# Optimization experiments

Hardware: AMD Instinct MI355X
Metric: run time of the kernel (lower is better)

## Reference

```python
import jax, jax.numpy as jnp
import numpy as np

_EPS = 1e-5
_I48 = float(1.0 / np.sqrt(48.0))
_I16 = float(1.0 / np.sqrt(16.0))
# fully-connected TP paths (mul_in, mul_out) for hidden(48x0e+48x1o+16x1e) x sh(0e+1e+2e) -> hidden
_PATHS = [(48, 48), (48, 16), (48, 48), (48, 48), (48, 48), (16, 16), (16, 48), (16, 16), (16, 16)]
_NW = sum(i * o for i, o in _PATHS)  # 11520


def _ln(x, g, b):
    mu = x.mean(-1, keepdims=True)
    var = ((x - mu) ** 2).mean(-1, keepdims=True)
    return g * (x - mu) * jax.lax.rsqrt(var + _EPS) + b


def _split(W):
    out, off = [], 0
    for i, o in _PATHS:
        out.append(W[:, off:off + i * o].reshape(-1, i, o))
        off += i * o
    return out


def _forward(protein_coords, protein_features, ligand_coords, ligand_features, t,
             te_w1, te_b1, te_w2, te_b2, te_ln_g, te_ln_b,
             pe_w1, pe_b1, pe_ln_g, pe_ln_b, pe_w2, pe_b2,
             le_w1, le_b1, le_ln_g, le_ln_b, le_w2, le_b2,
             sp_w, sp_b, emb_w, ee_w1, ee_b1, ee_w2, ee_b2,
             conv_w1, conv_b1, conv_w2, conv_b2, conv_w3, conv_b3,
             bn_gs, bn_bs, bn_gv, bn_gw, si_ws, si_wv, si_ww,
             out_ws, out_wv, edge_src, edge_dst):
    Nl = ligand_coords.shape[0]
    Np = protein_coords.shape[0]
    N = Nl + Np
    E = edge_src.shape[0]
    silu = jax.nn.silu

    # sinusoidal time embedding -> Linear/SiLU/Linear/LayerNorm
    half = 32
    freq = jnp.exp(jnp.arange(half, dtype=jnp.float32) * (-np.log(10000.0) / (half - 1)))
    emb = t[:, None] * freq[None, :]
    emb = jnp.concatenate([jnp.sin(emb), jnp.cos(emb)], -1)  # (1, 64)
    temb = _ln(silu(emb @ te_w1 + te_b1) @ te_w2 + te_b2, te_ln_g, te_ln_b)

    # scalar node encoders (dropout = eval identity)
    protein_ca = protein_coords[:, 0, :]
    ph = silu(_ln(protein_features @ pe_w1 + pe_b1, pe_ln_g, pe_ln_b)) @ pe_w2 + pe_b2
    lh = silu(_ln(ligand_features @ le_w1 + le_b1, le_ln_g, le_ln_b)) @ le_w2 + le_b2

    # edge geometry (ligand -> protein) + spherical harmonics in Cartesian form
    vec = ligand_coords[edge_src] - protein_ca[edge_dst]  # (E, 3)
    dist = jnp.sqrt((vec ** 2).sum(-1) + 1e-12)
    n = vec / dist[:, None]  # unit vector = l=1 SH
    Q = n[:, :, None] * n[:, None, :] - jnp.eye(3, dtype=n.dtype) / 3.0  # l=2 SH (traceless sym)
    te_exp = jnp.broadcast_to(temb[0], (E, temb.shape[-1]))
    ef = silu(jnp.concatenate([dist[:, None], te_exp], -1) @ ee_w1 + ee_b1) @ ee_w2 + ee_b2  # (E, 32)

    # input embedding: scalars only feed 0e; 1o/1e channels start at zero
    comb = jnp.concatenate([lh, ph], 0) @ sp_w + sp_b  # (N, 48)
    s = (comb @ emb_w) * _I48
    v = jnp.zeros((N, 48, 3), s.dtype)
    w = jnp.zeros((N, 16, 3), s.dtype)

    dst_n = edge_dst + Nl
    deg = jax.ops.segment_sum(jnp.ones((E,), s.dtype), dst_n, N).clip(1.0)

    for i in range(conv_w1.shape[0]):
        # edge MLP -> per-edge fully-connected tensor-product weights
        m = silu(ef @ conv_w1[i] + conv_b1[i])
        m = silu(m @ conv_w2[i] + conv_b2[i])
        Wt = m @ conv_w3[i] + conv_b3[i]  # (E, 11520)
        Wss, Wsw, Wv0, Wv1, Wv2, Ww0, Wws, Ww1, Ww2 = _split(Wt)

        se, ve, we = s[edge_src], v[edge_src], w[edge_src]
        wn = jnp.einsum('eid,ed->ei', we, n)        # 1e x 1e -> 0e (dot)
        cv = jnp.cross(ve, n[:, None, :])           # 1o x 1e -> 1o (cross)
        cw = jnp.cross(we, n[:, None, :])           # 1e x 1e -> 1e (cross)
        qv = jnp.einsum('edc,eic->eid', Q, ve)      # 1o x 2e -> 1o
        qw = jnp.einsum('edc,eic->eid', Q, we)      # 1e x 2e -> 1e

        m_s = jnp.einsum('eio,ei->eo', Wss, se) * _I48 + jnp.einsum('eio,ei->eo', Wws, wn) * _I16
        m_v = (jnp.einsum('eio,eid->eod', Wv0, ve) + jnp.einsum('eio,eid->eod', Wv1, cv)
               + jnp.einsum('eio,eid->eod', Wv2, qv)) * _I48
        m_w = jnp.einsum('eio,ei,ed->eod', Wsw, se, n) * _I48 + (
            jnp.einsum('eio,eid->eod', Ww0, we) + jnp.einsum('eio,eid->eod', Ww1, cw)
            + jnp.einsum('eio,eid->eod', Ww2, qw)) * _I16

        # scatter-mean to destination nodes
        S = jax.ops.segment_sum(m_s, dst_n, N) / deg[:, None]
        V = jax.ops.segment_sum(m_v, dst_n, N) / deg[:, None, None]
        Wm = jax.ops.segment_sum(m_w, dst_n, N) / deg[:, None, None]

        # self interaction (per-irrep linear)
        a_s = S + (s @ si_ws[i]) * _I48
        a_v = V + jnp.einsum('io,nid->nod', si_wv[i], v) * _I48
        a_w = Wm + jnp.einsum('io,nid->nod', si_ww[i], w) * _I16

        # equivariant batch norm (batch statistics)
        mu = a_s.mean(0)
        var = ((a_s - mu) ** 2).mean(0)
        n_s = bn_gs[i] * (a_s - mu) * jax.lax.rsqrt(var + _EPS) + bn_bs[i]
        n_v = a_v * (bn_gv[i] * jax.lax.rsqrt((a_v ** 2).sum(-1).mean(0) + _EPS))[None, :, None]
        n_w = a_w * (bn_gw[i] * jax.lax.rsqrt((a_w ** 2).sum(-1).mean(0) + _EPS))[None, :, None]

        s, v, w = s + n_s, v + n_v, w + n_w

    feats = (s[:Nl] @ out_ws) * _I48                          # (Nl, 256)
    out_v = jnp.einsum('io,nid->nod', out_wv, v[:Nl]) * _I48  # (Nl, 3, 3)
    vf = out_v.mean(1)                                        # vector_field (Nl, 3)
    return jnp.concatenate([vf, feats], -1)                   # (Nl, 259)


def setup_inputs():
    key = jax.random.key(0)
    ks = iter(jax.random.split(key, 80))
    f32 = jnp.float32

    def nrm(shape, scale=1.0):
        return jax.random.normal(next(ks), shape, f32) * scale

    def lin(fi, fo, lead=()):
        return nrm(lead + (fi, fo), 1.0 / np.sqrt(fi)), jnp.zeros(lead + (fo,), f32)

    Nl, Np, E, L = 2048, 4096, 8192, 6
    inp = {}
    inp['protein_coords'] = nrm((Np, 2, 3), 5.0)
    inp['protein_features'] = nrm((Np, 96))
    inp['ligand_coords'] = nrm((Nl, 3), 5.0)
    inp['ligand_features'] = nrm((Nl, 52))
    inp['t'] = jax.random.uniform(next(ks), (1,), f32)
    inp['te_w1'], inp['te_b1'] = lin(64, 128)
    inp['te_w2'], inp['te_b2'] = lin(128, 64)
    inp['te_ln_g'], inp['te_ln_b'] = jnp.ones((64,), f32), jnp.zeros((64,), f32)
    inp['pe_w1'], inp['pe_b1'] = lin(96, 128)
    inp['pe_ln_g'], inp['pe_ln_b'] = jnp.ones((128,), f32), jnp.zeros((128,), f32)
    inp['pe_w2'], inp['pe_b2'] = lin(128, 48)
    inp['le_w1'], inp['le_b1'] = lin(52, 128)
    inp['le_ln_g'], inp['le_ln_b'] = jnp.ones((128,), f32), jnp.zeros((128,), f32)
    inp['le_w2'], inp['le_b2'] = lin(128, 48)
    inp['sp_w'], inp['sp_b'] = lin(48, 48)
    inp['emb_w'] = nrm((48, 48))
    inp['ee_w1'], inp['ee_b1'] = lin(65, 32)
    inp['ee_w2'], inp['ee_b2'] = lin(32, 32)
    inp['conv_w1'], inp['conv_b1'] = lin(32, 128, (L,))
    inp['conv_w2'], inp['conv_b2'] = lin(128, 128, (L,))
    inp['conv_w3'], inp['conv_b3'] = lin(128, _NW, (L,))
    inp['bn_gs'], inp['bn_bs'] = jnp.ones((L, 48), f32), jnp.zeros((L, 48), f32)
    inp['bn_gv'], inp['bn_gw'] = jnp.ones((L, 48), f32), jnp.ones((L, 16), f32)
    inp['si_ws'] = nrm((L, 48, 48))
    inp['si_wv'] = nrm((L, 48, 48))
    inp['si_ww'] = nrm((L, 16, 16))
    inp['out_ws'] = nrm((48, 256))
    inp['out_wv'] = nrm((48, 3))
    inp['edge_src'] = jax.random.randint(next(ks), (E,), 0, Nl)
    inp['edge_dst'] = jax.random.randint(next(ks), (E,), 0, Np)
    return inp


def reference(protein_coords, protein_features, ligand_coords, ligand_features, t,
              te_w1, te_b1, te_w2, te_b2, te_ln_g, te_ln_b,
              pe_w1, pe_b1, pe_ln_g, pe_ln_b, pe_w2, pe_b2,
              le_w1, le_b1, le_ln_g, le_ln_b, le_w2, le_b2,
              sp_w, sp_b, emb_w, ee_w1, ee_b1, ee_w2, ee_b2,
              conv_w1, conv_b1, conv_w2, conv_b2, conv_w3, conv_b3,
              bn_gs, bn_bs, bn_gv, bn_gw, si_ws, si_wv, si_ww,
              out_ws, out_wv, edge_src, edge_dst):
    return _forward(protein_coords, protein_features, ligand_coords, ligand_features, t,
                    te_w1, te_b1, te_w2, te_b2, te_ln_g, te_ln_b,
                    pe_w1, pe_b1, pe_ln_g, pe_ln_b, pe_w2, pe_b2,
                    le_w1, le_b1, le_ln_g, le_ln_b, le_w2, le_b2,
                    sp_w, sp_b, emb_w, ee_w1, ee_b1, ee_w2, ee_b2,
                    conv_w1, conv_b1, conv_w2, conv_b2, conv_w3, conv_b3,
                    bn_gs, bn_bs, bn_gv, bn_gw, si_ws, si_wv, si_ww,
                    out_ws, out_wv, edge_src, edge_dst)
```

## Files before the change

kernel.cpp:

```cpp
#include <hip/hip_runtime.h>
#include <hip/hip_bf16.h>
#include <math.h>

#define I48 0.14433756729740643f
#define NKB 194
#define KCH 4
#define KSPL 6

typedef __attribute__((ext_vector_type(8))) _Float16 half8;
typedef __attribute__((ext_vector_type(4))) float f32x4;

__device__ __forceinline__ float silu_f(float x){ return x / (1.f + __expf(-x)); }

__global__ void k_temb(const float* __restrict__ t_in,
                       const float* __restrict__ w1, const float* __restrict__ b1,
                       const float* __restrict__ w2, const float* __restrict__ b2,
                       const float* __restrict__ g,  const float* __restrict__ b,
                       float* __restrict__ temb){
  __shared__ float emb[64], h1[128], red[128];
  __shared__ float s_mu, s_rs;
  int t = threadIdx.x;
  float tv = t_in[0];
  if (t < 64){
    int i = t & 31;
    float fr = __expf((float)i * (-9.210340371976184f/31.f));
    float a = tv * fr;
    emb[t] = (t < 32) ? sinf(a) : cosf(a);
  }
  __syncthreads();
  {
    float z = b1[t];
    for (int i=0;i<64;i++) z += emb[i]*w1[i*128+t];
    h1[t] = silu_f(z);
  }
  __syncthreads();
  float tp = 0.f;
  if (t < 64){
    tp = b2[t];
    for (int j=0;j<128;j++) tp += h1[j]*w2[j*64+t];
  }
  red[t] = (t<64)? tp : 0.f;
  __syncthreads();
  for (int st=64;st;st>>=1){ if(t<st) red[t]+=red[t+st]; __syncthreads(); }
  if (t==0) s_mu = red[0]/64.f;
  __syncthreads();
  float d = tp - s_mu;
  red[t] = (t<64)? d*d : 0.f;
  __syncthreads();
  for (int st=64;st;st>>=1){ if(t<st) red[t]+=red[t+st]; __syncthreads(); }
  if (t==0) s_rs = rsqrtf(red[0]/64.f + 1e-5f);
  __syncthreads();
  if (t<64) temb[t] = g[t]*(d*s_rs) + b[t];
}

__global__ void k_enc(const float* __restrict__ x, int in_dim,
                      const float* __restrict__ w1, const float* __restrict__ b1,
                      const float* __restrict__ g,  const float* __restrict__ bb,
                      const float* __restrict__ w2, const float* __restrict__ b2,
                      float* __restrict__ out, int row_off){
  __shared__ float sx[96], sh[128], red[128];
  __shared__ float s_mu, s_rs;
  int row = blockIdx.x, t = threadIdx.x;
  for (int i=t;i<in_dim;i+=128) sx[i] = x[(size_t)row*in_dim+i];
  __syncthreads();
  float z = b1[t];
  for (int i=0;i<in_dim;i++) z += sx[i]*w1[i*128+t];
  red[t]=z; __syncthreads();
  for (int st=64;st;st>>=1){ if(t<st) red[t]+=red[t+st]; __syncthreads(); }
  if(!t) s_mu = red[0]/128.f;
  __syncthreads();
  float d = z - s_mu;
  red[t]=d*d; __syncthreads();
  for (int st=64;st;st>>=1){ if(t<st) red[t]+=red[t+st]; __syncthreads(); }
  if(!t) s_rs = rsqrtf(red[0]/128.f+1e-5f);
  __syncthreads();
  float h = g[t]*(d*s_rs)+bb[t];
  sh[t] = silu_f(h);
  __syncthreads();
  if (t<48){
    float o = b2[t];
    for (int j=0;j<128;j++) o += sh[j]*w2[j*48+t];
    out[(size_t)(row_off+row)*48+t] = o;
  }
}

__global__ void k_s0(const float* __restrict__ enc, const float* __restrict__ spw,
                     const float* __restrict__ spb, const float* __restrict__ embw,
                     float* __restrict__ s){
  __shared__ float se[48], sc[48];
  int n = blockIdx.x, t = threadIdx.x;
  if (t<48) se[t] = enc[(size_t)n*48+t];
  __syncthreads();
  if (t<48){
    float c = spb[t];
    for (int i=0;i<48;i++) c += se[i]*spw[i*48+t];
    sc[t] = c;
  }
  __syncthreads();
  if (t<48){
    float v = 0.f;
    for (int i=0;i<48;i++) v += sc[i]*embw[i*48+t];
    s[(size_t)n*48+t] = v*I48;
  }
}

__global__ void k_edge(const float* __restrict__ lc, const float* __restrict__ pc,
                       const int* __restrict__ src, const int* __restrict__ dst,
                       const float* __restrict__ temb,
                       const float* __restrict__ w1, const float* __restrict__ b1,
                       const float* __restrict__ w2, const float* __restrict__ b2,
                       float* __restrict__ ef, float* __restrict__ degf,
                       int E, int Nl){
  __shared__ float sh_h[2][32];
  int t = threadIdx.x, sub = t>>5, j = t&31;
  int e = blockIdx.x*2 + sub;
  if (e < E){
    int s_ = src[e], d_ = dst[e];
    float vx = lc[(size_t)s_*3+0]-pc[(size_t)d_*6+0];
    float vy = lc[(size_t)s_*3+1]-pc[(size_t)d_*6+1];
    float vz = lc[(size_t)s_*3+2]-pc[(size_t)d_*6+2];
    float dist = sqrtf(vx*vx+vy*vy+vz*vz+1e-12f);
    float h = b1[j] + dist*w1[j];
    for (int a=0;a<64;a++) h += temb[a]*w1[(a+1)*32+j];
    sh_h[sub][j] = silu_f(h);
  }
  __syncthreads();
  if (e < E){
    float o = b2[j];
    for (int a=0;a<32;a++) o += sh_h[sub][a]*w2[a*32+j];
    ef[(size_t)e*32+j] = o;
    if (j==0) atomicAdd(&degf[Nl + dst[e]], 1.f);
  }
}

__global__ void k_packMLP(const float* __restrict__ w1, const float* __restrict__ w2,
                          _Float16* __restrict__ w1p, _Float16* __restrict__ w2p, int L){
  int tot1 = L*8*512;
  int tot2 = L*32*512;
  int total = tot1 + tot2;
  for (int idx = blockIdx.x*blockDim.x+threadIdx.x; idx < total; idx += gridDim.x*blockDim.x){
    if (idx < tot1){
      int j = idx & 7, lane = (idx>>3)&63, rest = idx>>9;
      int nt = rest & 7, l = rest >> 3;
      int k = (lane>>4)*8 + j, o = nt*16 + (lane&15);
      w1p[idx] = (_Float16)w1[((size_t)l*32 + k)*128 + o];
    } else {
      int i2 = idx - tot1;
      int j = i2 & 7, lane = (i2>>3)&63, rest = i2>>9;
      int nt = rest & 7, kb = (rest>>3)&3, l = rest >> 5;
      int k = kb*32 + (lane>>4)*8 + j, o = nt*16 + (lane&15);
      w2p[i2] = (_Float16)w2[((size_t)l*128 + k)*128 + o];
    }
  }
}

__global__ __launch_bounds__(256) void k_mlp2(
    const float* __restrict__ ef,
    const _Float16* __restrict__ w1p, const float* __restrict__ b1a,
    const _Float16* __restrict__ w2p, const float* __restrict__ b2a,
    _Float16* __restrict__ m2h, int E){
  __shared__ __align__(16) _Float16 sef[64][40];
  __shared__ __align__(16) _Float16 shh[64][136];
  __shared__ float sb1[128], sb2[128];
  const int t = threadIdx.x, lane = t & 63, w = t >> 6;
  const int e0 = blockIdx.x * 64;
  const int l  = blockIdx.y;
  const _Float16* w1l = w1p + (size_t)l*4096;
  const _Float16* w2l = w2p + (size_t)l*16384;
  if (t < 128) sb1[t] = b1a[l*128 + t];
  else         sb2[t-128] = b2a[l*128 + (t-128)];
  {
    int row = t >> 2, g = t & 3;
    const float* p = ef + ((size_t)(e0+row))*32 + g*8;
    float4 p0 = *(const float4*)p, p1 = *(const float4*)(p+4);
    half8 hv;
    hv[0]=(_Float16)p0.x; hv[1]=(_Float16)p0.y; hv[2]=(_Float16)p0.z; hv[3]=(_Float16)p0.w;
    hv[4]=(_Float16)p1.x; hv[5]=(_Float16)p1.y; hv[6]=(_Float16)p1.z; hv[7]=(_Float16)p1.w;
    *(half8*)&sef[row][g*8] = hv;
  }
  __syncthreads();
  const int m = lane & 15, quad = lane >> 4;
  const int r = w*16 + m;
  half8 a1 = *(const half8*)&sef[r][quad*8];
  f32x4 acc1[8];
  #pragma unroll
  for (int nt=0; nt<8; nt++){
    half8 b = *(const half8*)(w1l + (nt*64 + lane)*8);
    f32x4 z = {0.f,0.f,0.f,0.f};
    acc1[nt] = __builtin_amdgcn_mfma_f32_16x16x32_f16(a1, b, z, 0,0,0);
  }
  #pragma unroll
  for (int nt=0; nt<8; nt++){
    float bv = sb1[nt*16 + m];
    #pragma unroll
    for (int rr=0; rr<4; rr++)
      shh[w*16 + quad*4 + rr][nt*16 + m] = (_Float16)silu_f(acc1[nt][rr] + bv);
  }
  __syncthreads();
  f32x4 acc2[8];
  #pragma unroll
  for (int nt=0;nt<8;nt++) acc2[nt] = (f32x4){0.f,0.f,0.f,0.f};
  #pragma unroll
  for (int kb=0; kb<4; kb++){
    half8 a2 = *(const half8*)&shh[r][kb*32 + quad*8];
    #pragma unroll
    for (int nt=0; nt<8; nt++){
      half8 b = *(const half8*)(w2l + ((size_t)(kb*8+nt)*64 + lane)*8);
      acc2[nt] = __builtin_amdgcn_mfma_f32_16x16x32_f16(a2, b, acc2[nt], 0,0,0);
    }
  }
  __syncthreads();
  #pragma unroll
  for (int nt=0; nt<8; nt++){
    float bv = sb2[nt*16 + m];
    #pragma unroll
    for (int rr=0; rr<4; rr++)
      shh[w*16 + quad*4 + rr][nt*16 + m] = (_Float16)silu_f(acc2[nt][rr] + bv);
  }
  __syncthreads();
  for (int q = t; q < 64*16; q += 256){
    int row = q >> 4, c = q & 15;
    half8 hv = *(const half8*)&shh[row][c*8];
    *(half8*)(m2h + ((size_t)l*E + e0 + row)*128 + c*8) = hv;
  }
}

__global__ void k_packB(const float* __restrict__ w3, const float* __restrict__ b3,
                        _Float16* __restrict__ wbh, int L){
  int total = L*NKB*1536;
  for (int idx = blockIdx.x*blockDim.x+threadIdx.x; idx < total; idx += gridDim.x*blockDim.x){
    int j = idx & 7;
    int lane = (idx >> 3) & 63;
    int rest = idx >> 9;
    int nt = rest % 3; int rest2 = rest / 3;
    int kblk = rest2 % NKB; int l = rest2 / NKB;
    int kp = kblk*32 + ((lane>>4)<<3) + j;
    int o  = nt*16 + (lane & 15);
    float v;
    if (kp < 6144){
      int i = kp >> 7, kk = kp & 127;
      v = w3[((size_t)(l*128 + kk))*11520 + i*48 + o];
    } else {
      int ii = kp - 6144;
      v = (ii < 48) ? b3[(size_t)l*11520 + ii*48 + o] : 0.f;
    }
    wbh[idx] = (_Float16)v;
  }
}

__global__ __launch_bounds__(128) void k_msg3(
    const _Float16* __restrict__ m2h, const float* __restrict__ s,
    const _Float16* __restrict__ wbh,
    const int* __restrict__ src, const int* __restrict__ dst,
    float* __restrict__ Sacc, int Nl){
  __shared__ __align__(16) _Float16 sB[2][KCH*1536];
  __shared__ __align__(16) _Float16 sm2h[64][136];
  __shared__ __align__(16) _Float16 sseq[64][72];
  __shared__ int sdst[64];
  const int t = threadIdx.x, lane = t & 63, w = t >> 6;
  const int e0 = blockIdx.x * 64;
  const int by = blockIdx.y;
  const int kb0 = (NKB*by)/KSPL, kb1 = (NKB*(by+1))/KSPL;

  for (int q = t; q < 64*16; q += 128){
    int e = q >> 4, c = q & 15;
    float4 v = *(const float4*)(m2h + ((size_t)(e0+e))*128 + c*8);
    *(float4*)&sm2h[e][c*8] = v;
  }
  for (int q = t; q < 64*9; q += 128){
    int e = q/9, g = q - e*9;
    half8 hv = {};
    if (g < 6){
      const float* sp = s + (size_t)src[e0+e]*48 + g*8;
      float4 p0 = *(const float4*)sp, p1 = *(const float4*)(sp+4);
      hv[0]=(_Float16)p0.x; hv[1]=(_Float16)p0.y; hv[2]=(_Float16)p0.z; hv[3]=(_Float16)p0.w;
      hv[4]=(_Float16)p1.x; hv[5]=(_Float16)p1.y; hv[6]=(_Float16)p1.z; hv[7]=(_Float16)p1.w;
    }
    *(half8*)&sseq[e][g*8] = hv;
  }
  if (t < 64) sdst[t] = dst[e0+t];

  auto stage = [&](int c){
    int kbase = kb0 + c*KCH;
    int nk = kb1 - kbase; if (nk > KCH) nk = KCH;
    int bytes = nk*3072;
    const char* g = (const char*)wbh + (size_t)kbase*3072;
    char* lb = (char*)sB[c&1];
    for (int off = w*1024; off < bytes; off += 2048){
      __builtin_amdgcn_global_load_lds(
        (const __attribute__((address_space(1))) void*)(g + off + (size_t)lane*16),
        (__attribute__((address_space(3))) void*)(lb + off), 16, 0, 0);
    }
  };
  stage(0);

  const int m = lane & 15, quad = lane >> 4;
  const int r0 = w*32 + m, r1 = r0 + 16;
  f32x4 acc00={0.f,0.f,0.f,0.f}, acc01={0.f,0.f,0.f,0.f}, acc02={0.f,0.f,0.f,0.f};
  f32x4 acc10={0.f,0.f,0.f,0.f}, acc11={0.f,0.f,0.f,0.f}, acc12={0.f,0.f,0.f,0.f};

  const int nch = (kb1-kb0+KCH-1)/KCH;
  for (int c = 0; c < nch; c++){
    __syncthreads();
    if (c+1 < nch) stage(c+1);
    int kbase = kb0 + c*KCH;
    int kbn = kb1 - kbase; if (kbn > KCH) kbn = KCH;
    const _Float16* bb = sB[c&1];
    for (int kk = 0; kk < kbn; kk++){
      int kblk = kbase + kk;
      half8 a0, a1;
      if (kblk < 192){
        int i = kblk >> 2;
        int base = ((kblk & 3) << 5) + quad*8;
        _Float16 sv0 = sseq[r0][i], sv1 = sseq[r1][i];
        half8 m0 = *(const half8*)&sm2h[r0][base];
        half8 m1 = *(const half8*)&sm2h[r1][base];
        half8 s0v = {sv0,sv0,sv0,sv0,sv0,sv0,sv0,sv0};
        half8 s1v = {sv1,sv1,sv1,sv1,sv1,sv1,sv1,sv1};
        a0 = m0 * s0v;
        a1 = m1 * s1v;
      } else {
        int ib = ((kblk-192) << 5) + quad*8;
        a0 = *(const half8*)&sseq[r0][ib];
        a1 = *(const half8*)&sseq[r1][ib];
      }
      const _Float16* bk = bb + kk*1536 + lane*8;
      half8 b0 = *(const half8*)(bk);
      half8 b1 = *(const half8*)(bk + 512);
      half8 b2 = *(const half8*)(bk + 1024);
      acc00 = __builtin_amdgcn_mfma_f32_16x16x32_f16(a0, b0, acc00, 0, 0, 0);
      acc01 = __builtin_amdgcn_mfma_f32_16x16x32_f16(a0, b1, acc01, 0, 0, 0);
      acc02 = __builtin_amdgcn_mfma_f32_16x16x32_f16(a0, b2, acc02, 0, 0, 0);
      acc10 = __builtin_amdgcn_mfma_f32_16x16x32_f16(a1, b0, acc10, 0, 0, 0);
      acc11 = __builtin_amdgcn_mfma_f32_16x16x32_f16(a1, b1, acc11, 0, 0, 0);
      acc12 = __builtin_amdgcn_mfma_f32_16x16x32_f16(a1, b2, acc12, 0, 0, 0);
    }
  }
  #pragma unroll
  for (int r = 0; r < 4; r++){
    int el0 = w*32 + quad*4 + r;
    int el1 = el0 + 16;
    float* p0 = Sacc + (size_t)(Nl + sdst[el0])*48 + m;
    float* p1 = Sacc + (size_t)(Nl + sdst[el1])*48 + m;
    atomicAdd(p0 +  0, acc00[r]*I48);
    atomicAdd(p0 + 16, acc01[r]*I48);
    atomicAdd(p0 + 32, acc02[r]*I48);
    atomicAdd(p1 +  0, acc10[r]*I48);
    atomicAdd(p1 + 16, acc11[r]*I48);
    atomicAdd(p1 + 32, acc12[r]*I48);
  }
}

__global__ __launch_bounds__(256) void k_node(const float* __restrict__ Sacc,
                       const float* __restrict__ degf,
                       const float* __restrict__ s, const float* __restrict__ siw,
                       float* __restrict__ a_s, float* __restrict__ bnpart, int N){
  __shared__ float sh_s[16][48];
  __shared__ float sw[2304];
  __shared__ float csum[48], csq[48];
  int t = threadIdx.x;
  int n0 = blockIdx.x*16;
  for (int q=t;q<2304;q+=256) sw[q] = siw[q];
  for (int q=t;q<768;q+=256){
    int nl=q/48, i=q-nl*48;
    sh_s[nl][i] = s[(size_t)(n0+nl)*48+i];
  }
  if (t<48){ csum[t]=0.f; csq[t]=0.f; }
  __syncthreads();
  int nl = t>>4;
  int ob = (t&15)*3;
  int n = n0+nl;
  float dg = degf[n]; if (dg < 1.f) dg = 1.f;
  float inv = 1.f/dg;
  #pragma unroll
  for (int j=0;j<3;j++){
    int o = ob+j;
    float acc = 0.f;
    for (int i=0;i<48;i++) acc += sh_s[nl][i]*sw[i*48+o];
    float a = Sacc[(size_t)n*48+o]*inv + acc*I48;
    a_s[(size_t)n*48+o] = a;
    atomicAdd(&csum[o], a);
    atomicAdd(&csq[o], a*a);
  }
  __syncthreads();
  if (t<96) bnpart[(size_t)blockIdx.x*96 + t] = (t<48) ? csum[t] : csq[t-48];
}

__global__ void k_bnfin2(const float* __restrict__ bnpart,
                         const float* __restrict__ g, const float* __restrict__ b,
                         float* __restrict__ kscale, float* __restrict__ kbias,
                         int nblk, int N){
  __shared__ float red[8][96];
  __shared__ float tot[96];
  int t = threadIdx.x;
  int gg = t/96, o = t - gg*96;
  float acc = 0.f;
  for (int bk=gg; bk<nblk; bk+=8) acc += bnpart[(size_t)bk*96 + o];
  red[gg][o] = acc;
  __syncthreads();
  if (t<96){
    float s2 = 0.f;
    #pragma unroll
    for (int k=0;k<8;k++) s2 += red[k][t];
    tot[t] = s2;
  }
  __syncthreads();
  if (t<48){
    float mu  = tot[t]/(float)N;
    float var = tot[48+t]/(float)N - mu*mu;
    float r = rsqrtf(var + 1e-5f);
    float sc = g[t]*r;
    kscale[t] = sc;
    kbias[t]  = b[t] - mu*sc;
  }
}

__global__ void k_supd(float* __restrict__ s, float* __restrict__ Sacc,
                       const float* __restrict__ a_s,
                       const float* __restrict__ kscale, const float* __restrict__ kbias,
                       int total){
  int idx = blockIdx.x*blockDim.x+threadIdx.x;
  if (idx < total){
    int o = idx % 48;
    s[idx] += a_s[idx]*kscale[o] + kbias[o];
    Sacc[idx] = 0.f;
  }
}

__global__ void k_out(const float* __restrict__ s, const float* __restrict__ ows,
                      float* __restrict__ out){
  __shared__ float sh_s[48];
  int n = blockIdx.x, t = threadIdx.x;
  if (t<48) sh_s[t] = s[(size_t)n*48+t];
  __syncthreads();
  float acc = 0.f;
  for (int i=0;i<48;i++) acc += sh_s[i]*ows[i*256+t];
  out[(size_t)n*259 + 3 + t] = acc*I48;
  if (t<3) out[(size_t)n*259 + t] = 0.f;
}

extern "C" void kernel_launch(void* const* d_in, const int* in_sizes, int n_in,
                              void* d_out, int out_size, void* d_ws, size_t ws_size,
                              hipStream_t stream){
  const float* protein_coords   = (const float*)d_in[0];
  const float* protein_features = (const float*)d_in[1];
  const float* ligand_coords    = (const float*)d_in[2];
  const float* ligand_features  = (const float*)d_in[3];
  const float* t_in    = (const float*)d_in[4];
  const float* te_w1   = (const float*)d_in[5];
  const float* te_b1   = (const float*)d_in[6];
  const float* te_w2   = (const float*)d_in[7];
  const float* te_b2   = (const float*)d_in[8];
  const float* te_ln_g = (const float*)d_in[9];
  const float* te_ln_b = (const float*)d_in[10];
  const float* pe_w1   = (const float*)d_in[11];
  const float* pe_b1   = (const float*)d_in[12];
  const float* pe_ln_g = (const float*)d_in[13];
  const float* pe_ln_b = (const float*)d_in[14];
  const float* pe_w2   = (const float*)d_in[15];
  const float* pe_b2   = (const float*)d_in[16];
  const float* le_w1   = (const float*)d_in[17];
  const float* le_b1   = (const float*)d_in[18];
  const float* le_ln_g = (const float*)d_in[19];
  const float* le_ln_b = (const float*)d_in[20];
  const float* le_w2   = (const float*)d_in[21];
  const float* le_b2   = (const float*)d_in[22];
  const float* sp_w    = (const float*)d_in[23];
  const float* sp_b    = (const float*)d_in[24];
  const float* emb_w   = (const float*)d_in[25];
  const float* ee_w1   = (const float*)d_in[26];
  const float* ee_b1   = (const float*)d_in[27];
  const float* ee_w2   = (const float*)d_in[28];
  const float* ee_b2   = (const float*)d_in[29];
  const float* conv_w1 = (const float*)d_in[30];
  const float* conv_b1 = (const float*)d_in[31];
  const float* conv_w2 = (const float*)d_in[32];
  const float* conv_b2 = (const float*)d_in[33];
  const float* conv_w3 = (const float*)d_in[34];
  const float* conv_b3 = (const float*)d_in[35];
  const float* bn_gs   = (const float*)d_in[36];
  const float* bn_bs   = (const float*)d_in[37];
  const float* si_ws   = (const float*)d_in[40];
  const float* out_ws  = (const float*)d_in[43];
  const int* edge_src  = (const int*)d_in[45];
  const int* edge_dst  = (const int*)d_in[46];

  int Np = in_sizes[0]/6;
  int Nl = in_sizes[2]/3;
  int E  = in_sizes[45];
  int N  = Nl+Np;
  int L  = in_sizes[36]/48;

  float* W = (float*)d_ws;
  size_t off = 0;
  auto alloc = [&](size_t n)->float*{ float* p = W+off; off += (n+63)&~(size_t)63; return p; };
  float* temb  = alloc(64);
  float* enc   = alloc((size_t)N*48);
  float* sbuf  = alloc((size_t)N*48);
  float* ef    = alloc((size_t)E*32);
  float* degf  = alloc(N);
  float* Sacc  = alloc((size_t)N*48);
  float* a_s   = alloc((size_t)N*48);
  float* bnpart= alloc((size_t)(N/16)*96);
  float* kscale= alloc(64);
  float* kbias = alloc(64);
  _Float16* m2h = (_Float16*)alloc((size_t)L*E*128/2 + 64);
  _Float16* wbh = (_Float16*)alloc((size_t)L*NKB*1536/2 + 64);
  _Float16* w1p = (_Float16*)alloc((size_t)L*4096/2 + 64);
  _Float16* w2p = (_Float16*)alloc((size_t)L*16384/2 + 64);

  hipMemsetAsync(degf, 0, (size_t)N*sizeof(float), stream);
  hipMemsetAsync(Sacc, 0, (size_t)N*48*sizeof(float), stream);
  k_packB<<<1024,256,0,stream>>>(conv_w3, conv_b3, wbh, L);
  k_packMLP<<<480,256,0,stream>>>(conv_w1, conv_w2, w1p, w2p, L);
  k_temb<<<1,128,0,stream>>>(t_in, te_w1, te_b1, te_w2, te_b2, te_ln_g, te_ln_b, temb);
  k_enc<<<Np,128,0,stream>>>(protein_features, 96, pe_w1, pe_b1, pe_ln_g, pe_ln_b, pe_w2, pe_b2, enc, Nl);
  k_enc<<<Nl,128,0,stream>>>(ligand_features, 52, le_w1, le_b1, le_ln_g, le_ln_b, le_w2, le_b2, enc, 0);
  k_s0<<<N,64,0,stream>>>(enc, sp_w, sp_b, emb_w, sbuf);
  k_edge<<<(E+1)/2,64,0,stream>>>(ligand_coords, protein_coords, edge_src, edge_dst, temb,
                                  ee_w1, ee_b1, ee_w2, ee_b2, ef, degf, E, Nl);
  dim3 mlpg(E/64, L);
  k_mlp2<<<mlpg,256,0,stream>>>(ef, w1p, conv_b1, w2p, conv_b2, m2h, E);

  dim3 mgrid(E/64, KSPL);
  for (int l=0;l<L;l++){
    k_msg3<<<mgrid,128,0,stream>>>(m2h + (size_t)l*E*128, sbuf, wbh + (size_t)l*NKB*1536,
                                   edge_src, edge_dst, Sacc, Nl);
    k_node<<<N/16,256,0,stream>>>(Sacc, degf, sbuf, si_ws + (size_t)l*2304, a_s, bnpart, N);
    k_bnfin2<<<1,768,0,stream>>>(bnpart, bn_gs + l*48, bn_bs + l*48, kscale, kbias, N/16, N);
    k_supd<<<((size_t)N*48+255)/256,256,0,stream>>>(sbuf, Sacc, a_s, kscale, kbias, N*48);
  }
  k_out<<<Nl,256,0,stream>>>(sbuf, out_ws, (float*)d_out);
}
```

Baseline: 548.3 us.

## Enlarge message tile to 128 edges, fuse BN finalize into update, coalesce weight packing

The message kernel now processes 128 edges per block with 256 threads, so each staged weight chunk is reused across twice as many edges and total weight traffic drops. The BN finalize and state-update kernels are merged into one: every block re-reduces the per-block partial sums itself and then applies the update, removing one launch per layer at the cost of redundant reductions. The B-weight packing kernel now iterates in source order so reads are coalesced and writes are scattered. The larger tile halves the number of blocks and raises shared-memory use, which may reduce occupancy.

```diff
diff --git a/kernel.cpp b/kernel.cpp
--- a/kernel.cpp
+++ b/kernel.cpp
@@ -225,49 +225,58 @@
   }
 }
 
-__global__ void k_packB(const float* __restrict__ w3, const float* __restrict__ b3,
-                        _Float16* __restrict__ wbh, int L){
-  int total = L*NKB*1536;
+__global__ void k_packB2(const float* __restrict__ w3, const float* __restrict__ b3,
+                         _Float16* __restrict__ wbh, int L){
+  int tot1 = L*128*2304;
+  int tot2 = L*64*48;
+  int total = tot1 + tot2;
   for (int idx = blockIdx.x*blockDim.x+threadIdx.x; idx < total; idx += gridDim.x*blockDim.x){
-    int j = idx & 7;
-    int lane = (idx >> 3) & 63;
-    int rest = idx >> 9;
-    int nt = rest % 3; int rest2 = rest / 3;
-    int kblk = rest2 % NKB; int l = rest2 / NKB;
-    int kp = kblk*32 + ((lane>>4)<<3) + j;
-    int o  = nt*16 + (lane & 15);
-    float v;
-    if (kp < 6144){
-      int i = kp >> 7, kk = kp & 127;
-      v = w3[((size_t)(l*128 + kk))*11520 + i*48 + o];
+    if (idx < tot1){
+      int r = idx % 2304; int q = idx / 2304;
+      int kk = q & 127;   int l = q >> 7;
+      float v = w3[(size_t)(l*128+kk)*11520 + r];
+      int i = r / 48, o = r - i*48;
+      int kp = i*128 + kk;
+      int kblk = kp >> 5, p = kp & 31;
+      int lane = ((p>>3)<<4) + (o & 15);
+      int j = p & 7;
+      int nt = o >> 4;
+      wbh[((((size_t)l*NKB + kblk)*3 + nt)*64 + lane)*8 + j] = (_Float16)v;
     } else {
-      int ii = kp - 6144;
-      v = (ii < 48) ? b3[(size_t)l*11520 + ii*48 + o] : 0.f;
+      int i2 = idx - tot1;
+      int o = i2 % 48; int q = i2 / 48;
+      int ii = q & 63; int l = q >> 6;
+      float v = (ii < 48) ? b3[(size_t)l*11520 + ii*48 + o] : 0.f;
+      int kp = 6144 + ii;
+      int kblk = kp >> 5, p = kp & 31;
+      int lane = ((p>>3)<<4) + (o & 15);
+      int j = p & 7;
+      int nt = o >> 4;
+      wbh[((((size_t)l*NKB + kblk)*3 + nt)*64 + lane)*8 + j] = (_Float16)v;
     }
-    wbh[idx] = (_Float16)v;
-  }
-}
-
-__global__ __launch_bounds__(128) void k_msg3(
+  }
+}
+
+__global__ __launch_bounds__(256) void k_msg4(
     const _Float16* __restrict__ m2h, const float* __restrict__ s,
     const _Float16* __restrict__ wbh,
     const int* __restrict__ src, const int* __restrict__ dst,
     float* __restrict__ Sacc, int Nl){
   __shared__ __align__(16) _Float16 sB[2][KCH*1536];
-  __shared__ __align__(16) _Float16 sm2h[64][136];
-  __shared__ __align__(16) _Float16 sseq[64][72];
-  __shared__ int sdst[64];
+  __shared__ __align__(16) _Float16 sm2h[128][136];
+  __shared__ __align__(16) _Float16 sseq[128][72];
+  __shared__ int sdst[128];
   const int t = threadIdx.x, lane = t & 63, w = t >> 6;
-  const int e0 = blockIdx.x * 64;
+  const int e0 = blockIdx.x * 128;
   const int by = blockIdx.y;
   const int kb0 = (NKB*by)/KSPL, kb1 = (NKB*(by+1))/KSPL;
 
-  for (int q = t; q < 64*16; q += 128){
+  for (int q = t; q < 128*16; q += 256){
     int e = q >> 4, c = q & 15;
     float4 v = *(const float4*)(m2h + ((size_t)(e0+e))*128 + c*8);
     *(float4*)&sm2h[e][c*8] = v;
   }
-  for (int q = t; q < 64*9; q += 128){
+  for (int q = t; q < 128*9; q += 256){
     int e = q/9, g = q - e*9;
     half8 hv = {};
     if (g < 6){
@@ -278,7 +287,7 @@
     }
     *(half8*)&sseq[e][g*8] = hv;
   }
-  if (t < 64) sdst[t] = dst[e0+t];
+  if (t < 128) sdst[t] = dst[e0+t];
 
   auto stage = [&](int c){
     int kbase = kb0 + c*KCH;
@@ -286,7 +295,7 @@
     int bytes = nk*3072;
     const char* g = (const char*)wbh + (size_t)kbase*3072;
     char* lb = (char*)sB[c&1];
-    for (int off = w*1024; off < bytes; off += 2048){
+    for (int off = w*1024; off < bytes; off += 4096){
       __builtin_amdgcn_global_load_lds(
         (const __attribute__((address_space(1))) void*)(g + off + (size_t)lane*16),
         (__attribute__((address_space(3))) void*)(lb + off), 16, 0, 0);
@@ -386,43 +395,37 @@
   if (t<96) bnpart[(size_t)blockIdx.x*96 + t] = (t<48) ? csum[t] : csq[t-48];
 }
 
-__global__ void k_bnfin2(const float* __restrict__ bnpart,
-                         const float* __restrict__ g, const float* __restrict__ b,
-                         float* __restrict__ kscale, float* __restrict__ kbias,
-                         int nblk, int N){
-  __shared__ float red[8][96];
-  __shared__ float tot[96];
+__global__ __launch_bounds__(256) void k_supd2(
+    float* __restrict__ s, float* __restrict__ Sacc,
+    const float* __restrict__ a_s, const float* __restrict__ bnpart,
+    const float* __restrict__ g, const float* __restrict__ b,
+    int nblk, int N){
+  __shared__ float red[2][96];
+  __shared__ float ksc[48], kbs[48];
   int t = threadIdx.x;
-  int gg = t/96, o = t - gg*96;
-  float acc = 0.f;
-  for (int bk=gg; bk<nblk; bk+=8) acc += bnpart[(size_t)bk*96 + o];
-  red[gg][o] = acc;
-  __syncthreads();
-  if (t<96){
-    float s2 = 0.f;
-    #pragma unroll
-    for (int k=0;k<8;k++) s2 += red[k][t];
-    tot[t] = s2;
-  }
-  __syncthreads();
-  if (t<48){
-    float mu  = tot[t]/(float)N;
-    float var = tot[48+t]/(float)N - mu*mu;
+  if (t < 192){
+    int gg = t/96, o = t - gg*96;
+    float acc = 0.f;
+    for (int bk=gg; bk<nblk; bk+=2) acc += bnpart[(size_t)bk*96 + o];
+    red[gg][o] = acc;
+  }
+  __syncthreads();
+  if (t < 48){
+    float su = red[0][t] + red[1][t];
+    float sq = red[0][48+t] + red[1][48+t];
+    float mu  = su/(float)N;
+    float var = sq/(float)N - mu*mu;
     float r = rsqrtf(var + 1e-5f);
     float sc = g[t]*r;
-    kscale[t] = sc;
-    kbias[t]  = b[t] - mu*sc;
-  }
-}
-
-__global__ void k_supd(float* __restrict__ s, float* __restrict__ Sacc,
-                       const float* __restrict__ a_s,
-                       const float* __restrict__ kscale, const float* __restrict__ kbias,
-                       int total){
-  int idx = blockIdx.x*blockDim.x+threadIdx.x;
-  if (idx < total){
-    int o = idx % 48;
-    s[idx] += a_s[idx]*kscale[o] + kbias[o];
+    ksc[t] = sc;
+    kbs[t] = b[t] - mu*sc;
+  }
+  __syncthreads();
+  int n0 = blockIdx.x*16;
+  for (int q=t; q<768; q+=256){
+    int o = q % 48;
+    size_t idx = (size_t)n0*48 + q;
+    s[idx] += a_s[idx]*ksc[o] + kbs[o];
     Sacc[idx] = 0.f;
   }
 }
@@ -508,10 +511,11 @@
   _Float16* wbh = (_Float16*)alloc((size_t)L*NKB*1536/2 + 64);
   _Float16* w1p = (_Float16*)alloc((size_t)L*4096/2 + 64);
   _Float16* w2p = (_Float16*)alloc((size_t)L*16384/2 + 64);
+  (void)kscale; (void)kbias;
 
   hipMemsetAsync(degf, 0, (size_t)N*sizeof(float), stream);
   hipMemsetAsync(Sacc, 0, (size_t)N*48*sizeof(float), stream);
-  k_packB<<<1024,256,0,stream>>>(conv_w3, conv_b3, wbh, L);
+  k_packB2<<<2048,256,0,stream>>>(conv_w3, conv_b3, wbh, L);
   k_packMLP<<<480,256,0,stream>>>(conv_w1, conv_w2, w1p, w2p, L);
   k_temb<<<1,128,0,stream>>>(t_in, te_w1, te_b1, te_w2, te_b2, te_ln_g, te_ln_b, temb);
   k_enc<<<Np,128,0,stream>>>(protein_features, 96, pe_w1, pe_b1, pe_ln_g, pe_ln_b, pe_w2, pe_b2, enc, Nl);
@@ -522,13 +526,12 @@
   dim3 mlpg(E/64, L);
   k_mlp2<<<mlpg,256,0,stream>>>(ef, w1p, conv_b1, w2p, conv_b2, m2h, E);
 
-  dim3 mgrid(E/64, KSPL);
+  dim3 mgrid(E/128, KSPL);
   for (int l=0;l<L;l++){
-    k_msg3<<<mgrid,128,0,stream>>>(m2h + (size_t)l*E*128, sbuf, wbh + (size_t)l*NKB*1536,
+    k_msg4<<<mgrid,256,0,stream>>>(m2h + (size_t)l*E*128, sbuf, wbh + (size_t)l*NKB*1536,
                                    edge_src, edge_dst, Sacc, Nl);
     k_node<<<N/16,256,0,stream>>>(Sacc, degf, sbuf, si_ws + (size_t)l*2304, a_s, bnpart, N);
-    k_bnfin2<<<1,768,0,stream>>>(bnpart, bn_gs + l*48, bn_bs + l*48, kscale, kbias, N/16, N);
-    k_supd<<<((size_t)N*48+255)/256,256,0,stream>>>(sbuf, Sacc, a_s, kscale, kbias, N*48);
+    k_supd2<<<N/16,256,0,stream>>>(sbuf, Sacc, a_s, bnpart, bn_gs + l*48, bn_bs + l*48, N/16, N);
   }
   k_out<<<Nl,256,0,stream>>>(sbuf, out_ws, (float*)d_out);
 }
```

Result: slower. 744.1 us (+35.7%).
